# Optimization experiments

Hardware: AMD Instinct MI355X
Metric: run time of the kernel (lower is better)

Reference implementation:

```python
import jax, jax.numpy as jnp
import numpy as np

SAMPLE_RATE = 0.25  # nsample = SAMPLE_RATE * points_num, as in get_indexes


def setup_inputs() -> dict:
    key = jax.random.key(0)
    k1, k2 = jax.random.split(key)
    xyz = jax.random.normal(k1, (32, 16384, 3), dtype=jnp.float32)
    feat = jax.random.normal(k2, (32, 16384, 128), dtype=jnp.float32)
    return {"xyz": xyz, "feat": feat}


def farthest_point_sample(xyz, nsample):
    """Iterative FPS: at each step pick the point farthest from the selected set.
    xyz: [B, N, 3] -> indexes [B, nsample] (int32). Deterministic start at index 0."""
    B, N, _ = xyz.shape

    def step(carry, _):
        dist, farthest = carry  # dist: [B, N] min sq-dist to selected set; farthest: [B]
        centroid = jnp.take_along_axis(xyz, farthest[:, None, None], axis=1)  # [B,1,3]
        d = jnp.sum((xyz - centroid) ** 2, axis=-1)  # [B, N]
        dist = jnp.minimum(dist, d)
        nxt = jnp.argmax(dist, axis=-1).astype(jnp.int32)
        return (dist, nxt), farthest

    init = (jnp.full((B, N), jnp.finfo(xyz.dtype).max, xyz.dtype),
            jnp.zeros((B,), jnp.int32))
    _, idx = jax.lax.scan(step, init, None, length=nsample)  # [nsample, B]
    return idx.T  # [B, nsample]


def index_points(points, idx):
    """points: [B, N, C], idx: [B, S] -> [B, S, C] (torch index_points gather)."""
    return jnp.take_along_axis(points, idx[..., None], axis=1)


def reference(xyz, feat):
    points_num = xyz.shape[1]
    nsample = int(SAMPLE_RATE * points_num)
    sample_indexes = farthest_point_sample(xyz, nsample)  # [B, nsample]
    sampled_xyz = index_points(xyz, sample_indexes)       # [B, nsample, 3]
    sampled_feat = index_points(feat, sample_indexes)     # [B, nsample, C]
    return sampled_xyz, sampled_feat
```

## Files before the change

### kernel.cpp

```cpp
#include <hip/hip_runtime.h>
#include <hip/hip_bf16.h>
#include <cfloat>


#define FPS_THREADS 512

#define REP32(M) M(0) M(1) M(2) M(3) M(4) M(5) M(6) M(7) \
                 M(8) M(9) M(10) M(11) M(12) M(13) M(14) M(15) \
                 M(16) M(17) M(18) M(19) M(20) M(21) M(22) M(23) \
                 M(24) M(25) M(26) M(27) M(28) M(29) M(30) M(31)

__global__ __launch_bounds__(FPS_THREADS) void transpose_kernel(
    const float* __restrict__ xyz, float2* __restrict__ xyp,
    float* __restrict__ zp, int N) {
  const int b = blockIdx.x;
  const int t = threadIdx.x;
  const float* xb = xyz + (size_t)b * N * 3;
  float2* xyb = xyp + (size_t)b * N;
  float* zb = zp + (size_t)b * N;
#pragma unroll
  for (int k = 0; k < 32; ++k) {
    int p = k * FPS_THREADS + t;
    xyb[p] = make_float2(xb[(size_t)p * 3 + 0], xb[(size_t)p * 3 + 1]);
    zb[p] = xb[(size_t)p * 3 + 2];
  }
}

__global__ __launch_bounds__(FPS_THREADS, 2)
void fps_kernel(const float2* __restrict__ xyp, const float* __restrict__ zp,
                int* __restrict__ out_idx, int N, int S) {
#pragma clang fp contract(off)
  const int b = blockIdx.x;
  const int t = threadIdx.x;
  const float2* xyb = xyp + (size_t)b * N;
  const float* zb = zp + (size_t)b * N;

#define DECLP(k) float ds##k;
  REP32(DECLP)
#define INITP(k) ds##k = FLT_MAX;
  REP32(INITP)

  __shared__ unsigned long long s_k[2][FPS_THREADS / 64];

  const int wave = t >> 6;
  const int lane = t & 63;
  const unsigned invt = 0xFFFFFFFFu - (unsigned)t;
  int farthest = 0;

  for (int s = 0; s < S; ++s) {
    if (t == 0) out_idx[(size_t)b * S + s] = farthest;

    int f = __builtin_amdgcn_readfirstlane(farthest);
    float2 cxy = xyb[f];
    float cz = zb[f];
    float cx = cxy.x, cy = cxy.y;

    float bestv = -1.0f;
    int bestk = 0;

#define STEPP(k) {                                               \
    int p = (k) * FPS_THREADS + t;                               \
    float2 xy = xyb[p];                                          \
    float dz = zb[p] - cz;                                       \
    float dx = xy.x - cx;                                        \
    float dy = xy.y - cy;                                        \
    float y2 = dy * dy;                                          \
    float inner = __builtin_fmaf(dx, dx, y2);                    \
    float dd = __builtin_fmaf(dz, dz, inner);                    \
    float nd = fminf(ds##k, dd);                                 \
    ds##k = nd;                                                  \
    if (nd > bestv) { bestv = nd; bestk = (k); } }
    REP32(STEPP)

    unsigned bestinv = invt - (unsigned)(bestk * FPS_THREADS);
    unsigned long long bestkkey =
        ((unsigned long long)__float_as_uint(bestv) << 32) |
        (unsigned long long)bestinv;

#pragma unroll
    for (int off = 32; off > 0; off >>= 1) {
      unsigned long long ok = __shfl_xor(bestkkey, off, 64);
      if (ok > bestkkey) bestkkey = ok;
    }

    const int par = s & 1;
    if (lane == 0) s_k[par][wave] = bestkkey;
    __syncthreads();

    unsigned long long bk = s_k[par][0];
#pragma unroll
    for (int w = 1; w < FPS_THREADS / 64; ++w) {
      unsigned long long ok = s_k[par][w];
      if (ok > bk) bk = ok;
    }
    farthest = (int)(0xFFFFFFFFu - (unsigned)(bk & 0xFFFFFFFFu));
  }
}

__global__ void gather_kernel(const float* __restrict__ xyz,
                              const float* __restrict__ feat,
                              const int* __restrict__ idx,
                              float* __restrict__ out,
                              int B, int N, int S, int C) {
  const int c4pr = C >> 2;
  const int nf4 = B * S * c4pr;
  int tid = blockIdx.x * blockDim.x + threadIdx.x;
  if (tid < nf4) {
    int c4 = tid % c4pr;
    int bs = tid / c4pr;
    int s = bs % S, b = bs / S;
    int p = idx[b * S + s];
    const float4* src = (const float4*)(feat + ((size_t)b * N + p) * C);
    float4* dst = (float4*)(out + (size_t)B * S * 3 + ((size_t)bs) * C);
    dst[c4] = src[c4];
  } else {
    int t2 = tid - nf4;
    int nxyz = B * S * 3;
    if (t2 < nxyz) {
      int c = t2 % 3;
      int bs = t2 / 3;
      int s = bs % S, b = bs / S;
      int p = idx[b * S + s];
      out[t2] = xyz[((size_t)b * N + p) * 3 + c];
    }
  }
}

extern "C" void kernel_launch(void* const* d_in, const int* in_sizes, int n_in,
                              void* d_out, int out_size, void* d_ws, size_t ws_size,
                              hipStream_t stream) {
  const float* xyz = (const float*)d_in[0];
  const float* feat = (const float*)d_in[1];
  float* out = (float*)d_out;

  const int B = 32;
  const int N = in_sizes[0] / (B * 3);
  const int C = in_sizes[1] / (B * N);
  const int S = N / 4;

  int* d_idx = (int*)d_ws;
  float2* d_xy = (float2*)((char*)d_ws + (size_t)B * S * sizeof(int));
  float* d_z = (float*)((char*)d_xy + (size_t)B * N * sizeof(float2));

  transpose_kernel<<<B, FPS_THREADS, 0, stream>>>(xyz, d_xy, d_z, N);
  fps_kernel<<<B, FPS_THREADS, 0, stream>>>(d_xy, d_z, d_idx, N, S);

  int total = B * S * (C >> 2) + B * S * 3;
  int blocks = (total + 255) / 256;
  gather_kernel<<<blocks, 256, 0, stream>>>(xyz, feat, d_idx, out, B, N, S, C);
}
```

Before: 5.979 ms.

## Stage FPS xy coordinates in LDS, process point pairs, use DPP wave reductions

The FPS kernel now copies each batch's xy coordinates into a 128 KB shared-memory array once. The serial sampling loop then reads them as float4 from LDS instead of re-reading global memory on every iteration. Each thread handles two adjacent points per load, and z is fetched as float2 from global. The 64-bit shuffle-based wave argmax is replaced by two 32-bit DPP max reductions: first the value, then the inverted index among lanes holding that maximum. The aim is to cut per-iteration load latency and reduction cost on the latency-bound serial loop. The cost is very high LDS use per block and more complex index bookkeeping.

```diff
diff --git a/kernel.cpp b/kernel.cpp
--- a/kernel.cpp
+++ b/kernel.cpp
@@ -5,10 +5,38 @@
 
 #define FPS_THREADS 512
 
-#define REP32(M) M(0) M(1) M(2) M(3) M(4) M(5) M(6) M(7) \
-                 M(8) M(9) M(10) M(11) M(12) M(13) M(14) M(15) \
-                 M(16) M(17) M(18) M(19) M(20) M(21) M(22) M(23) \
-                 M(24) M(25) M(26) M(27) M(28) M(29) M(30) M(31)
+#define REP16(M) M(0) M(1) M(2) M(3) M(4) M(5) M(6) M(7) \
+                 M(8) M(9) M(10) M(11) M(12) M(13) M(14) M(15)
+
+template <int CTRL>
+__device__ __forceinline__ float dpp_maxf(float v) {
+  int iv = __float_as_int(v);
+  int sh = __builtin_amdgcn_update_dpp(iv, iv, CTRL, 0xF, 0xF, false);
+  return fmaxf(v, __int_as_float(sh));
+}
+template <int CTRL>
+__device__ __forceinline__ unsigned dpp_maxu(unsigned v) {
+  int sh = __builtin_amdgcn_update_dpp((int)v, (int)v, CTRL, 0xF, 0xF, false);
+  return ((unsigned)sh > v) ? (unsigned)sh : v;
+}
+__device__ __forceinline__ float wave_maxf(float v) {
+  v = dpp_maxf<0xB1>(v);
+  v = dpp_maxf<0x4E>(v);
+  v = dpp_maxf<0x141>(v);
+  v = dpp_maxf<0x140>(v);
+  v = dpp_maxf<0x142>(v);
+  v = dpp_maxf<0x143>(v);
+  return __int_as_float(__builtin_amdgcn_readlane(__float_as_int(v), 63));
+}
+__device__ __forceinline__ unsigned wave_maxu(unsigned v) {
+  v = dpp_maxu<0xB1>(v);
+  v = dpp_maxu<0x4E>(v);
+  v = dpp_maxu<0x141>(v);
+  v = dpp_maxu<0x140>(v);
+  v = dpp_maxu<0x142>(v);
+  v = dpp_maxu<0x143>(v);
+  return (unsigned)__builtin_amdgcn_readlane((int)v, 63);
+}
 
 __global__ __launch_bounds__(FPS_THREADS) void transpose_kernel(
     const float* __restrict__ xyz, float2* __restrict__ xyp,
@@ -32,59 +60,71 @@
 #pragma clang fp contract(off)
   const int b = blockIdx.x;
   const int t = threadIdx.x;
-  const float2* xyb = xyp + (size_t)b * N;
+  const float4* xyb4 = (const float4*)(xyp + (size_t)b * N);
+  const float2* zb2 = (const float2*)(zp + (size_t)b * N);
   const float* zb = zp + (size_t)b * N;
 
-#define DECLP(k) float ds##k;
-  REP32(DECLP)
-#define INITP(k) ds##k = FLT_MAX;
-  REP32(INITP)
+  __shared__ float4 s_xy4[8192];
+  __shared__ unsigned long long s_k[2][FPS_THREADS / 64];
 
-  __shared__ unsigned long long s_k[2][FPS_THREADS / 64];
+#define DECLP(k) float dsA##k, dsB##k;
+  REP16(DECLP)
+
+#define LOADP(k) { int e = (k) * FPS_THREADS + t;  \
+    s_xy4[e] = xyb4[e];                            \
+    dsA##k = FLT_MAX; dsB##k = FLT_MAX; }
+  REP16(LOADP)
 
   const int wave = t >> 6;
   const int lane = t & 63;
-  const unsigned invt = 0xFFFFFFFFu - (unsigned)t;
+  const unsigned invt2 = 0xFFFFFFFFu - (unsigned)(2 * t);
   int farthest = 0;
+
+  __syncthreads();
 
   for (int s = 0; s < S; ++s) {
     if (t == 0) out_idx[(size_t)b * S + s] = farthest;
 
     int f = __builtin_amdgcn_readfirstlane(farthest);
-    float2 cxy = xyb[f];
     float cz = zb[f];
-    float cx = cxy.x, cy = cxy.y;
+    float4 cq = s_xy4[(f >> 10) * FPS_THREADS + ((f & 1023) >> 1)];
+    int j = f & 1;
+    float cx = j ? cq.z : cq.x;
+    float cy = j ? cq.w : cq.y;
 
     float bestv = -1.0f;
-    int bestk = 0;
+    int bestk = 0, bestj = 0;
 
 #define STEPP(k) {                                               \
-    int p = (k) * FPS_THREADS + t;                               \
-    float2 xy = xyb[p];                                          \
-    float dz = zb[p] - cz;                                       \
-    float dx = xy.x - cx;                                        \
-    float dy = xy.y - cy;                                        \
-    float y2 = dy * dy;                                          \
-    float inner = __builtin_fmaf(dx, dx, y2);                    \
-    float dd = __builtin_fmaf(dz, dz, inner);                    \
-    float nd = fminf(ds##k, dd);                                 \
-    ds##k = nd;                                                  \
-    if (nd > bestv) { bestv = nd; bestk = (k); } }
-    REP32(STEPP)
+    int e = (k) * FPS_THREADS + t;                               \
+    float4 q = s_xy4[e];                                         \
+    float2 z2 = zb2[e];                                          \
+    { float dx = q.x - cx, dy = q.y - cy, dz = z2.x - cz;        \
+      float y2 = dy * dy;                                        \
+      float inner = __builtin_fmaf(dx, dx, y2);                  \
+      float dd = __builtin_fmaf(dz, dz, inner);                  \
+      float nd = fminf(dsA##k, dd);                              \
+      dsA##k = nd;                                               \
+      if (nd > bestv) { bestv = nd; bestk = (k); bestj = 0; } }  \
+    { float dx = q.z - cx, dy = q.w - cy, dz = z2.y - cz;        \
+      float y2 = dy * dy;                                        \
+      float inner = __builtin_fmaf(dx, dx, y2);                  \
+      float dd = __builtin_fmaf(dz, dz, inner);                  \
+      float nd = fminf(dsB##k, dd);                              \
+      dsB##k = nd;                                               \
+      if (nd > bestv) { bestv = nd; bestk = (k); bestj = 1; } } }
+    REP16(STEPP)
 
-    unsigned bestinv = invt - (unsigned)(bestk * FPS_THREADS);
-    unsigned long long bestkkey =
-        ((unsigned long long)__float_as_uint(bestv) << 32) |
-        (unsigned long long)bestinv;
+    unsigned bestinv = invt2 - (unsigned)((bestk << 10) + bestj);
 
-#pragma unroll
-    for (int off = 32; off > 0; off >>= 1) {
-      unsigned long long ok = __shfl_xor(bestkkey, off, 64);
-      if (ok > bestkkey) bestkkey = ok;
-    }
+    float wmax = wave_maxf(bestv);
+    unsigned cand = (bestv == wmax) ? bestinv : 0u;
+    unsigned winv = wave_maxu(cand);
 
     const int par = s & 1;
-    if (lane == 0) s_k[par][wave] = bestkkey;
+    if (lane == 0)
+      s_k[par][wave] = ((unsigned long long)__float_as_uint(wmax) << 32) |
+                       (unsigned long long)winv;
     __syncthreads();
 
     unsigned long long bk = s_k[par][0];
```

After: 5.697 ms. 4.7% less time.

## Split each batch's FPS across 8 cooperative blocks with global-memory handshake

Applied to the files above, without the earlier changes.

Each batch's farthest point sampling now runs on 8 workgroups instead of one, launched as a cooperative kernel. Each workgroup holds 4 points per thread in registers rather than 32 and re-reading them from memory. Every step, the workgroups exchange their candidate argmax through global atomics with sequence-number spin waits. The wave reduction now uses DPP max operations. This spreads the serial per-batch work over more CUs, at the cost of a cross-workgroup synchronisation latency on every one of the 4096 steps.

```diff
diff --git a/kernel.cpp b/kernel.cpp
--- a/kernel.cpp
+++ b/kernel.cpp
@@ -4,11 +4,32 @@
 
 
 #define FPS_THREADS 512
-
-#define REP32(M) M(0) M(1) M(2) M(3) M(4) M(5) M(6) M(7) \
-                 M(8) M(9) M(10) M(11) M(12) M(13) M(14) M(15) \
-                 M(16) M(17) M(18) M(19) M(20) M(21) M(22) M(23) \
-                 M(24) M(25) M(26) M(27) M(28) M(29) M(30) M(31)
+#define PARTS 8
+#define PPT 4
+
+typedef unsigned long long u64;
+
+template <int CTRL>
+__device__ __forceinline__ float dpp_maxf(float v) {
+  int iv = __float_as_int(v);
+  int sh = __builtin_amdgcn_update_dpp(iv, iv, CTRL, 0xF, 0xF, false);
+  return fmaxf(v, __int_as_float(sh));
+}
+template <int CTRL>
+__device__ __forceinline__ unsigned dpp_maxu(unsigned v) {
+  int sh = __builtin_amdgcn_update_dpp((int)v, (int)v, CTRL, 0xF, 0xF, false);
+  return ((unsigned)sh > v) ? (unsigned)sh : v;
+}
+__device__ __forceinline__ float wave_maxf(float v) {
+  v = dpp_maxf<0xB1>(v); v = dpp_maxf<0x4E>(v); v = dpp_maxf<0x141>(v);
+  v = dpp_maxf<0x140>(v); v = dpp_maxf<0x142>(v); v = dpp_maxf<0x143>(v);
+  return __int_as_float(__builtin_amdgcn_readlane(__float_as_int(v), 63));
+}
+__device__ __forceinline__ unsigned wave_maxu(unsigned v) {
+  v = dpp_maxu<0xB1>(v); v = dpp_maxu<0x4E>(v); v = dpp_maxu<0x141>(v);
+  v = dpp_maxu<0x140>(v); v = dpp_maxu<0x142>(v); v = dpp_maxu<0x143>(v);
+  return (unsigned)__builtin_amdgcn_readlane((int)v, 63);
+}
 
 __global__ __launch_bounds__(FPS_THREADS) void transpose_kernel(
     const float* __restrict__ xyz, float2* __restrict__ xyp,
@@ -26,29 +47,37 @@
   }
 }
 
-__global__ __launch_bounds__(FPS_THREADS, 2)
+__global__ __launch_bounds__(FPS_THREADS)
 void fps_kernel(const float2* __restrict__ xyp, const float* __restrict__ zp,
-                int* __restrict__ out_idx, int N, int S) {
+                int* __restrict__ out_idx, u64* __restrict__ candbuf,
+                unsigned* __restrict__ seqbuf, int N, int S) {
 #pragma clang fp contract(off)
-  const int b = blockIdx.x;
+  const int b = blockIdx.x >> 3;
+  const int part = blockIdx.x & 7;
   const int t = threadIdx.x;
   const float2* xyb = xyp + (size_t)b * N;
   const float* zb = zp + (size_t)b * N;
-
-#define DECLP(k) float ds##k;
-  REP32(DECLP)
-#define INITP(k) ds##k = FLT_MAX;
-  REP32(INITP)
-
-  __shared__ unsigned long long s_k[2][FPS_THREADS / 64];
-
+  u64* cb = candbuf + (size_t)b * 16;
+  unsigned* sb = seqbuf + (size_t)b * 16;
+
+  const int base = part * (N / PARTS);
+  float px[PPT], py[PPT], pz[PPT], ds[PPT];
+#pragma unroll
+  for (int k = 0; k < PPT; ++k) {
+    int p = base + k * FPS_THREADS + t;
+    float2 xy = xyb[p];
+    px[k] = xy.x; py[k] = xy.y; pz[k] = zb[p];
+    ds[k] = FLT_MAX;
+  }
+
+  __shared__ u64 s_k[FPS_THREADS / 64];
+  __shared__ int s_far;
   const int wave = t >> 6;
   const int lane = t & 63;
-  const unsigned invt = 0xFFFFFFFFu - (unsigned)t;
   int farthest = 0;
 
   for (int s = 0; s < S; ++s) {
-    if (t == 0) out_idx[(size_t)b * S + s] = farthest;
+    if (part == 0 && t == 0) out_idx[(size_t)b * S + s] = farthest;
 
     int f = __builtin_amdgcn_readfirstlane(farthest);
     float2 cxy = xyb[f];
@@ -57,43 +86,58 @@
 
     float bestv = -1.0f;
     int bestk = 0;
-
-#define STEPP(k) {                                               \
-    int p = (k) * FPS_THREADS + t;                               \
-    float2 xy = xyb[p];                                          \
-    float dz = zb[p] - cz;                                       \
-    float dx = xy.x - cx;                                        \
-    float dy = xy.y - cy;                                        \
-    float y2 = dy * dy;                                          \
-    float inner = __builtin_fmaf(dx, dx, y2);                    \
-    float dd = __builtin_fmaf(dz, dz, inner);                    \
-    float nd = fminf(ds##k, dd);                                 \
-    ds##k = nd;                                                  \
-    if (nd > bestv) { bestv = nd; bestk = (k); } }
-    REP32(STEPP)
-
-    unsigned bestinv = invt - (unsigned)(bestk * FPS_THREADS);
-    unsigned long long bestkkey =
-        ((unsigned long long)__float_as_uint(bestv) << 32) |
-        (unsigned long long)bestinv;
-
-#pragma unroll
-    for (int off = 32; off > 0; off >>= 1) {
-      unsigned long long ok = __shfl_xor(bestkkey, off, 64);
-      if (ok > bestkkey) bestkkey = ok;
+#pragma unroll
+    for (int k = 0; k < PPT; ++k) {
+      float dx = px[k] - cx;
+      float dy = py[k] - cy;
+      float dz = pz[k] - cz;
+      float y2 = dy * dy;
+      float inner = __builtin_fmaf(dx, dx, y2);
+      float dd = __builtin_fmaf(dz, dz, inner);
+      float nd = fminf(ds[k], dd);
+      ds[k] = nd;
+      if (nd > bestv) { bestv = nd; bestk = k; }
     }
-
-    const int par = s & 1;
-    if (lane == 0) s_k[par][wave] = bestkkey;
+    unsigned bestinv = 0xFFFFFFFFu - (unsigned)(base + bestk * FPS_THREADS + t);
+
+    float wmax = wave_maxf(bestv);
+    unsigned cand = (bestv == wmax) ? bestinv : 0u;
+    unsigned winv = wave_maxu(cand);
+    if (lane == 0)
+      s_k[wave] = ((u64)__float_as_uint(wmax) << 32) | (u64)winv;
     __syncthreads();
 
-    unsigned long long bk = s_k[par][0];
-#pragma unroll
-    for (int w = 1; w < FPS_THREADS / 64; ++w) {
-      unsigned long long ok = s_k[par][w];
-      if (ok > bk) bk = ok;
+    if (wave == 0) {
+      u64 kk = s_k[lane & 7];
+#pragma unroll
+      for (int off = 1; off < 8; off <<= 1) {
+        u64 ok = __shfl_xor(kk, off, 64);
+        if (ok > kk) kk = ok;
+      }
+      const int par = s & 1;
+      if (lane == 0) {
+        __hip_atomic_store(&cb[par * 8 + part], kk,
+                           __ATOMIC_RELAXED, __HIP_MEMORY_SCOPE_AGENT);
+        __hip_atomic_store(&sb[par * 8 + part], (unsigned)(s + 1),
+                           __ATOMIC_RELEASE, __HIP_MEMORY_SCOPE_AGENT);
+      }
+      u64 gk = 0;
+      if (lane < 8) {
+        while (__hip_atomic_load(&sb[par * 8 + lane], __ATOMIC_ACQUIRE,
+                                 __HIP_MEMORY_SCOPE_AGENT) < (unsigned)(s + 1)) {}
+        gk = __hip_atomic_load(&cb[par * 8 + lane], __ATOMIC_RELAXED,
+                               __HIP_MEMORY_SCOPE_AGENT);
+      }
+#pragma unroll
+      for (int off = 1; off < 8; off <<= 1) {
+        u64 ok = __shfl_xor(gk, off, 64);
+        if (ok > gk) gk = ok;
+      }
+      if (lane == 0)
+        s_far = (int)(0xFFFFFFFFu - (unsigned)(gk & 0xFFFFFFFFu));
     }
-    farthest = (int)(0xFFFFFFFFu - (unsigned)(bk & 0xFFFFFFFFu));
+    __syncthreads();
+    farthest = s_far;
   }
 }
 
@@ -141,9 +185,19 @@
   int* d_idx = (int*)d_ws;
   float2* d_xy = (float2*)((char*)d_ws + (size_t)B * S * sizeof(int));
   float* d_z = (float*)((char*)d_xy + (size_t)B * N * sizeof(float2));
-
+  u64* d_cand = (u64*)((char*)d_z + (size_t)B * N * sizeof(float));
+  unsigned* d_seq = (unsigned*)((char*)d_cand + (size_t)B * 16 * sizeof(u64));
+
+  hipMemsetAsync(d_seq, 0, (size_t)B * 16 * sizeof(unsigned), stream);
   transpose_kernel<<<B, FPS_THREADS, 0, stream>>>(xyz, d_xy, d_z, N);
-  fps_kernel<<<B, FPS_THREADS, 0, stream>>>(d_xy, d_z, d_idx, N, S);
+
+  int* idxp = d_idx; const float2* xyp = d_xy; const float* zp = d_z;
+  u64* candp = d_cand; unsigned* seqp = d_seq; int n = N, ss = S;
+  void* args[] = {(void*)&xyp, (void*)&zp, (void*)&idxp,
+                  (void*)&candp, (void*)&seqp, (void*)&n, (void*)&ss};
+  hipLaunchCooperativeKernel((const void*)fps_kernel,
+                             dim3(B * PARTS), dim3(FPS_THREADS),
+                             args, 0, stream);
 
   int total = B * S * (C >> 2) + B * S * 3;
   int blocks = (total + 255) / 256;
```

Result: slower. 22.86 ms (+282.3%).
